# Kernel tuning notes

Hardware: AMD Instinct MI355X
Metric: run time of the kernel (lower is better)

## Reference

```python
import jax, jax.numpy as jnp
import numpy as np

M = 8192          # sketch width
TAU = 64.0
D = 3             # Chebyshev order
SIGMA_DP = 0.01


def setup_inputs() -> dict:
    key = jax.random.key(0)
    ks = jax.random.split(key, 8)
    B, C, K = 512, 4096, 1000
    x = jax.random.normal(ks[0], (B, C), dtype=jnp.float32)
    sketch_mu = jax.random.normal(ks[1], (C, M), dtype=jnp.float32) * 0.1
    g = jnp.where(jax.random.uniform(ks[2], (C,)) < 0.5, -1.0, 1.0).astype(jnp.float32)
    noise = jax.random.normal(ks[3], (C, M), dtype=jnp.float32)
    W = jax.random.normal(ks[4], (C, K), dtype=jnp.float32) * 0.02
    b = jax.random.normal(ks[5], (K,), dtype=jnp.float32) * 0.02
    h = jax.random.randint(ks[6], (C,), 0, M, dtype=jnp.int32)
    t = 10
    return {"x": x, "sketch_mu": sketch_mu, "g": g, "noise": noise,
            "W": W, "b": b, "h": h, "t": t}


def reference(x, sketch_mu, g, noise, W, b, h, t):
    tf = jnp.float32(t)
    lambda_t = 1.0 - jnp.exp(-tf / TAU)
    kappa_t = 1.0 / tf
    # hashed count-sketch scatter-add, vectorized over the batch:
    # per sample i: sketch_mu[:, h] += kappa * (g * x[i])[:, None]
    # under add semantics == kappa * outer(g * sum_i x[i], bincount(h))
    counts = jnp.zeros((M,), dtype=x.dtype).at[h].add(1.0)        # [m]
    update = kappa_t * (g * x.sum(axis=0))[:, None] * counts[None, :]  # [C, m]
    sk = sketch_mu * (1.0 - lambda_t) + update + SIGMA_DP * noise
    # moment estimation
    mu_hat = jnp.mean(sk * g[:, None], axis=1)                    # [C]
    var_hat = jnp.ones_like(mu_hat)
    skew_hat = jnp.zeros_like(mu_hat)
    kurt_hat = jnp.full_like(mu_hat, 3.0)
    # Chebyshev normalization (d = 3 -> all branches active)
    xn = (x - mu_hat) / (jnp.sqrt(var_hat) + 1e-6)
    if D >= 2:
        xn = xn - 0.5 * skew_hat * (xn ** 2 - 1.0)
    if D >= 3:
        xn = xn / jnp.sqrt(kurt_hat / 8.0 + 1e-6)
    # classifier head
    return xn @ W + b
```

## Files before the change

kernel.cpp:

```cpp
#include <hip/hip_runtime.h>
#include <hip/hip_bf16.h>


#define SPLITK 8

typedef float f32x4 __attribute__((ext_vector_type(4)));
typedef short bf16x8 __attribute__((ext_vector_type(8)));

__device__ __forceinline__ short f2bf(float f) {
    unsigned u = __float_as_uint(f);
    unsigned r = (u + 0x7FFFu + ((u >> 16) & 1u)) >> 16;
    return (short)r;
}
__device__ __forceinline__ float bf2f(short b) {
    return __uint_as_float(((unsigned)(unsigned short)b) << 16);
}

__global__ __launch_bounds__(256) void colsum_kernel(const float* __restrict__ x,
                                                     float* __restrict__ colsum,
                                                     int Cdim) {
    int c = blockIdx.x * 256 + threadIdx.x;
    const float* p = x + (size_t)(blockIdx.y * 8) * Cdim + c;
    float r0 = p[0 * (size_t)Cdim];
    float r1 = p[1 * (size_t)Cdim];
    float r2 = p[2 * (size_t)Cdim];
    float r3 = p[3 * (size_t)Cdim];
    float r4 = p[4 * (size_t)Cdim];
    float r5 = p[5 * (size_t)Cdim];
    float r6 = p[6 * (size_t)Cdim];
    float r7 = p[7 * (size_t)Cdim];
    __builtin_amdgcn_sched_barrier(0);
    float acc = ((r0 + r1) + (r2 + r3)) + ((r4 + r5) + (r6 + r7));
    atomicAdd(&colsum[c], acc);
}

__global__ __launch_bounds__(256, 4) void rowsum_kernel(const float* __restrict__ sk,
                                                        const float* __restrict__ noise,
                                                        const float* __restrict__ g,
                                                        const float* __restrict__ colsum,
                                                        const int* __restrict__ t_ptr,
                                                        float* __restrict__ mu,
                                                        int Msk, float hcount) {
    int row = blockIdx.x;
    int tid = threadIdx.x;
    const f32x4* ps = reinterpret_cast<const f32x4*>(sk + (size_t)row * Msk);
    const f32x4* pn = reinterpret_cast<const f32x4*>(noise + (size_t)row * Msk);
    int n4 = Msk >> 2;

    float ss = 0.0f, sn = 0.0f;
    int base = 0;
    for (; base + 2048 <= n4; base += 2048) {
        const f32x4* qs = ps + base + tid;
        const f32x4* qn = pn + base + tid;
        f32x4 a0 = __builtin_nontemporal_load(qs + 0 * 256);
        f32x4 a1 = __builtin_nontemporal_load(qs + 1 * 256);
        f32x4 a2 = __builtin_nontemporal_load(qs + 2 * 256);
        f32x4 a3 = __builtin_nontemporal_load(qs + 3 * 256);
        f32x4 a4 = __builtin_nontemporal_load(qs + 4 * 256);
        f32x4 a5 = __builtin_nontemporal_load(qs + 5 * 256);
        f32x4 a6 = __builtin_nontemporal_load(qs + 6 * 256);
        f32x4 a7 = __builtin_nontemporal_load(qs + 7 * 256);
        f32x4 b0 = __builtin_nontemporal_load(qn + 0 * 256);
        f32x4 b1 = __builtin_nontemporal_load(qn + 1 * 256);
        f32x4 b2 = __builtin_nontemporal_load(qn + 2 * 256);
        f32x4 b3 = __builtin_nontemporal_load(qn + 3 * 256);
        f32x4 b4 = __builtin_nontemporal_load(qn + 4 * 256);
        f32x4 b5 = __builtin_nontemporal_load(qn + 5 * 256);
        f32x4 b6 = __builtin_nontemporal_load(qn + 6 * 256);
        f32x4 b7 = __builtin_nontemporal_load(qn + 7 * 256);
        __builtin_amdgcn_sched_barrier(0);
        float s0 = (a0.x + a0.y) + (a0.z + a0.w);
        float s1 = (a1.x + a1.y) + (a1.z + a1.w);
        float s2 = (a2.x + a2.y) + (a2.z + a2.w);
        float s3 = (a3.x + a3.y) + (a3.z + a3.w);
        float s4 = (a4.x + a4.y) + (a4.z + a4.w);
        float s5 = (a5.x + a5.y) + (a5.z + a5.w);
        float s6 = (a6.x + a6.y) + (a6.z + a6.w);
        float s7 = (a7.x + a7.y) + (a7.z + a7.w);
        float t0 = (b0.x + b0.y) + (b0.z + b0.w);
        float t1 = (b1.x + b1.y) + (b1.z + b1.w);
        float t2 = (b2.x + b2.y) + (b2.z + b2.w);
        float t3 = (b3.x + b3.y) + (b3.z + b3.w);
        float t4 = (b4.x + b4.y) + (b4.z + b4.w);
        float t5 = (b5.x + b5.y) + (b5.z + b5.w);
        float t6 = (b6.x + b6.y) + (b6.z + b6.w);
        float t7 = (b7.x + b7.y) + (b7.z + b7.w);
        ss += ((s0 + s1) + (s2 + s3)) + ((s4 + s5) + (s6 + s7));
        sn += ((t0 + t1) + (t2 + t3)) + ((t4 + t5) + (t6 + t7));
    }
    for (int i = base + tid; i < n4; i += 256) {
        f32x4 v = ps[i];
        f32x4 w = pn[i];
        ss += (v.x + v.y) + (v.z + v.w);
        sn += (w.x + w.y) + (w.z + w.w);
    }

#pragma unroll
    for (int off = 32; off > 0; off >>= 1) {
        ss += __shfl_down(ss, off);
        sn += __shfl_down(sn, off);
    }
    __shared__ float red[2][4];
    int wid = tid >> 6;
    if ((tid & 63) == 0) { red[0][wid] = ss; red[1][wid] = sn; }
    __syncthreads();
    if (tid == 0) {
        float sst = (red[0][0] + red[0][1]) + (red[0][2] + red[0][3]);
        float snt = (red[1][0] + red[1][1]) + (red[1][2] + red[1][3]);
        float t = (float)(*t_ptr);
        float decay = __expf(-t / 64.0f);
        float kappa = 1.0f / t;
        float gc = g[row];
        float acc = decay * sst + 0.01f * snt;
        mu[row] = gc / (float)Msk * (acc + kappa * gc * colsum[row] * hcount);
    }
}

__global__ __launch_bounds__(256) void init_out_kernel(const float* __restrict__ bias,
                                                       float* __restrict__ out,
                                                       int Kdim, int total) {
    int i = blockIdx.x * 256 + threadIdx.x;
    if (i < total) out[i] = bias[i % Kdim];
}

template <bool ATOMIC>
__global__ __launch_bounds__(256, 4) void gemm_kernel(const float* __restrict__ x,
                                                      const float* __restrict__ W,
                                                      const float* __restrict__ mu,
                                                      float* __restrict__ outp,
                                                      int Bdim, int Cdim, int Kdim,
                                                      int Kc, float s) {
    __shared__ short As[2][64][40];
    __shared__ short Bs[2][64][40];

    const int tid = threadIdx.x;
    const int lane = tid & 63;
    const int w = tid >> 6;
    const int wr = w >> 1;
    const int wc = w & 1;
    const int row0 = blockIdx.x * 64;
    const int col0 = blockIdx.y * 64;
    const int cbeg = blockIdx.z * Kc;

    const int am = tid >> 2;
    const int ac8 = (tid & 3) * 8;
    const int bn = tid & 63;
    const int bk8 = (tid >> 6) * 8;
    const int bcol = col0 + bn;
    const bool bok = bcol < Kdim;

    const int fr = lane & 15;
    const int fk8 = (lane >> 4) * 8;

    f32x4 acc[2][2] = {};

    for (int it = 0; it < Kc; it += 32) {
        const int c0 = cbeg + it;
        const float* xr = &x[(size_t)(row0 + am) * Cdim + c0 + ac8];
        f32x4 xa = *reinterpret_cast<const f32x4*>(xr);
        f32x4 xb = *reinterpret_cast<const f32x4*>(xr + 4);
        f32x4 ma = *reinterpret_cast<const f32x4*>(&mu[c0 + ac8]);
        f32x4 mb = *reinterpret_cast<const f32x4*>(&mu[c0 + ac8 + 4]);
        float wv[8];
#pragma unroll
        for (int j = 0; j < 8; ++j)
            wv[j] = bok ? W[(size_t)(c0 + bk8 + j) * Kdim + bcol] : 0.0f;

        __syncthreads();

        float av[8];
        av[0] = s * (xa.x - ma.x); av[1] = s * (xa.y - ma.y);
        av[2] = s * (xa.z - ma.z); av[3] = s * (xa.w - ma.w);
        av[4] = s * (xb.x - mb.x); av[5] = s * (xb.y - mb.y);
        av[6] = s * (xb.z - mb.z); av[7] = s * (xb.w - mb.w);
        bf16x8 ah, al;
#pragma unroll
        for (int j = 0; j < 8; ++j) {
            short h = f2bf(av[j]);
            ah[j] = h;
            al[j] = f2bf(av[j] - bf2f(h));
        }
        *reinterpret_cast<bf16x8*>(&As[0][am][ac8]) = ah;
        *reinterpret_cast<bf16x8*>(&As[1][am][ac8]) = al;

        bf16x8 bh, bl;
#pragma unroll
        for (int j = 0; j < 8; ++j) {
            short h = f2bf(wv[j]);
            bh[j] = h;
            bl[j] = f2bf(wv[j] - bf2f(h));
        }
        *reinterpret_cast<bf16x8*>(&Bs[0][bn][bk8]) = bh;
        *reinterpret_cast<bf16x8*>(&Bs[1][bn][bk8]) = bl;

        __syncthreads();

        bf16x8 afr[2][2], bfr[2][2];
#pragma unroll
        for (int h = 0; h < 2; ++h) {
#pragma unroll
            for (int f = 0; f < 2; ++f) {
                afr[h][f] = *reinterpret_cast<const bf16x8*>(
                    &As[h][wr * 32 + f * 16 + fr][fk8]);
                bfr[h][f] = *reinterpret_cast<const bf16x8*>(
                    &Bs[h][wc * 32 + f * 16 + fr][fk8]);
            }
        }

#pragma unroll
        for (int mf = 0; mf < 2; ++mf) {
#pragma unroll
            for (int nf = 0; nf < 2; ++nf) {
                acc[mf][nf] = __builtin_amdgcn_mfma_f32_16x16x32_bf16(
                    afr[0][mf], bfr[0][nf], acc[mf][nf], 0, 0, 0);
                acc[mf][nf] = __builtin_amdgcn_mfma_f32_16x16x32_bf16(
                    afr[0][mf], bfr[1][nf], acc[mf][nf], 0, 0, 0);
                acc[mf][nf] = __builtin_amdgcn_mfma_f32_16x16x32_bf16(
                    afr[1][mf], bfr[0][nf], acc[mf][nf], 0, 0, 0);
            }
        }
    }

#pragma unroll
    for (int mf = 0; mf < 2; ++mf) {
#pragma unroll
        for (int nf = 0; nf < 2; ++nf) {
#pragma unroll
            for (int r = 0; r < 4; ++r) {
                int row = row0 + wr * 32 + mf * 16 + (lane >> 4) * 4 + r;
                int col = col0 + wc * 32 + nf * 16 + (lane & 15);
                if (col < Kdim) {
                    if (ATOMIC)
                        atomicAdd(&outp[(size_t)row * Kdim + col], acc[mf][nf][r]);
                    else
                        outp[((size_t)blockIdx.z * Bdim + row) * Kdim + col] =
                            acc[mf][nf][r];
                }
            }
        }
    }
}

__global__ __launch_bounds__(256) void reduce_kernel(const float* __restrict__ part,
                                                     const float* __restrict__ bias,
                                                     float* __restrict__ out,
                                                     int total4, int Kdim, int perz) {
    int i = blockIdx.x * 256 + threadIdx.x;
    if (i >= total4) return;
    const float4* p4 = reinterpret_cast<const float4*>(part);
    float4 sum = p4[i];
#pragma unroll
    for (int z = 1; z < SPLITK; ++z) {
        float4 v = p4[(size_t)z * (perz >> 2) + i];
        sum.x += v.x; sum.y += v.y; sum.z += v.z; sum.w += v.w;
    }
    int e = i * 4;
    sum.x += bias[(e + 0) % Kdim];
    sum.y += bias[(e + 1) % Kdim];
    sum.z += bias[(e + 2) % Kdim];
    sum.w += bias[(e + 3) % Kdim];
    reinterpret_cast<float4*>(out)[i] = sum;
}

extern "C" void kernel_launch(void* const* d_in, const int* in_sizes, int n_in,
                              void* d_out, int out_size, void* d_ws, size_t ws_size,
                              hipStream_t stream) {
    const float* x      = (const float*)d_in[0];
    const float* sk     = (const float*)d_in[1];
    const float* g      = (const float*)d_in[2];
    const float* noise  = (const float*)d_in[3];
    const float* W      = (const float*)d_in[4];
    const float* bias   = (const float*)d_in[5];
    const int* t_ptr    = (const int*)d_in[7];

    int C    = in_sizes[2];
    int Bdim = in_sizes[0] / C;
    int Msk  = in_sizes[1] / C;
    int Kdim = in_sizes[5];
    float hcount = (float)in_sizes[6];

    float* colsum = (float*)d_ws;
    float* mu     = colsum + C;
    float* part   = mu + C;

    size_t need = (size_t)(2 * C + SPLITK * Bdim * Kdim) * sizeof(float);
    bool use_partial = ws_size >= need;

    float s = (float)(1.0 / ((1.0 + 1e-6) * sqrt(0.375 + 1e-6)));
    int Kc = C / SPLITK;

    hipMemsetAsync(colsum, 0, C * sizeof(float), stream);
    {
        dim3 grid(C / 256, Bdim / 8);
        colsum_kernel<<<grid, 256, 0, stream>>>(x, colsum, C);
    }
    rowsum_kernel<<<C, 256, 0, stream>>>(sk, noise, g, colsum, t_ptr, mu, Msk, hcount);
    dim3 ggrid(Bdim / 64, (Kdim + 63) / 64, SPLITK);
    if (use_partial) {
        gemm_kernel<false><<<ggrid, 256, 0, stream>>>(x, W, mu, part, Bdim, C, Kdim,
                                                      Kc, s);
        int perz = Bdim * Kdim;
        int total4 = perz / 4;
        reduce_kernel<<<(total4 + 255) / 256, 256, 0, stream>>>(part, bias,
                                                                (float*)d_out,
                                                                total4, Kdim, perz);
    } else {
        int total = Bdim * Kdim;
        init_out_kernel<<<(total + 255) / 256, 256, 0, stream>>>(bias, (float*)d_out,
                                                                 Kdim, total);
        gemm_kernel<true><<<ggrid, 256, 0, stream>>>(x, W, mu, (float*)d_out, Bdim, C,
                                                     Kdim, Kc, s);
    }
}
```

Baseline: 313.3 us.

## Decouple mean subtraction from GEMM via GEMV and pre-split bf16 operands

Rewrites the normalized GEMM as s*(x@W) - s*(mu@W) + b, so mu now enters through a separate GEMV folded into the final reduce. This lets x and W be split into bf16 hi/lo once, in standalone kernels, instead of inside the GEMM inner loop. The rowsum is also split across two grid slices, one for the sketch and one for the noise, combined by atomics, to raise parallelism. The cost is extra workspace traffic and launches, and a slight change in rounding from subtracting mu after the product.

```diff
diff --git a/kernel.cpp b/kernel.cpp
--- a/kernel.cpp
+++ b/kernel.cpp
@@ -14,6 +14,25 @@
 }
 __device__ __forceinline__ float bf2f(short b) {
     return __uint_as_float(((unsigned)(unsigned short)b) << 16);
+}
+
+__global__ __launch_bounds__(256) void split_kernel(const float* __restrict__ src,
+                                                    short* __restrict__ hi,
+                                                    short* __restrict__ lo) {
+    int i = blockIdx.x * 256 + threadIdx.x;
+    const f32x4* p = reinterpret_cast<const f32x4*>(src) + 2 * (size_t)i;
+    f32x4 a = p[0];
+    f32x4 b = p[1];
+    float v[8] = {a.x, a.y, a.z, a.w, b.x, b.y, b.z, b.w};
+    bf16x8 h, l;
+#pragma unroll
+    for (int j = 0; j < 8; ++j) {
+        short hh = f2bf(v[j]);
+        h[j] = hh;
+        l[j] = f2bf(v[j] - bf2f(hh));
+    }
+    reinterpret_cast<bf16x8*>(hi)[i] = h;
+    reinterpret_cast<bf16x8*>(lo)[i] = l;
 }
 
 __global__ __launch_bounds__(256) void colsum_kernel(const float* __restrict__ x,
@@ -36,38 +55,27 @@
 
 __global__ __launch_bounds__(256, 4) void rowsum_kernel(const float* __restrict__ sk,
                                                         const float* __restrict__ noise,
-                                                        const float* __restrict__ g,
-                                                        const float* __restrict__ colsum,
                                                         const int* __restrict__ t_ptr,
-                                                        float* __restrict__ mu,
-                                                        int Msk, float hcount) {
+                                                        float* __restrict__ accrow,
+                                                        int Msk) {
     int row = blockIdx.x;
     int tid = threadIdx.x;
-    const f32x4* ps = reinterpret_cast<const f32x4*>(sk + (size_t)row * Msk);
-    const f32x4* pn = reinterpret_cast<const f32x4*>(noise + (size_t)row * Msk);
+    const float* src = (blockIdx.y == 0) ? sk : noise;
+    const f32x4* p = reinterpret_cast<const f32x4*>(src + (size_t)row * Msk);
     int n4 = Msk >> 2;
 
-    float ss = 0.0f, sn = 0.0f;
+    float sum = 0.0f;
     int base = 0;
     for (; base + 2048 <= n4; base += 2048) {
-        const f32x4* qs = ps + base + tid;
-        const f32x4* qn = pn + base + tid;
-        f32x4 a0 = __builtin_nontemporal_load(qs + 0 * 256);
-        f32x4 a1 = __builtin_nontemporal_load(qs + 1 * 256);
-        f32x4 a2 = __builtin_nontemporal_load(qs + 2 * 256);
-        f32x4 a3 = __builtin_nontemporal_load(qs + 3 * 256);
-        f32x4 a4 = __builtin_nontemporal_load(qs + 4 * 256);
-        f32x4 a5 = __builtin_nontemporal_load(qs + 5 * 256);
-        f32x4 a6 = __builtin_nontemporal_load(qs + 6 * 256);
-        f32x4 a7 = __builtin_nontemporal_load(qs + 7 * 256);
-        f32x4 b0 = __builtin_nontemporal_load(qn + 0 * 256);
-        f32x4 b1 = __builtin_nontemporal_load(qn + 1 * 256);
-        f32x4 b2 = __builtin_nontemporal_load(qn + 2 * 256);
-        f32x4 b3 = __builtin_nontemporal_load(qn + 3 * 256);
-        f32x4 b4 = __builtin_nontemporal_load(qn + 4 * 256);
-        f32x4 b5 = __builtin_nontemporal_load(qn + 5 * 256);
-        f32x4 b6 = __builtin_nontemporal_load(qn + 6 * 256);
-        f32x4 b7 = __builtin_nontemporal_load(qn + 7 * 256);
+        const f32x4* q = p + base + tid;
+        f32x4 a0 = __builtin_nontemporal_load(q + 0 * 256);
+        f32x4 a1 = __builtin_nontemporal_load(q + 1 * 256);
+        f32x4 a2 = __builtin_nontemporal_load(q + 2 * 256);
+        f32x4 a3 = __builtin_nontemporal_load(q + 3 * 256);
+        f32x4 a4 = __builtin_nontemporal_load(q + 4 * 256);
+        f32x4 a5 = __builtin_nontemporal_load(q + 5 * 256);
+        f32x4 a6 = __builtin_nontemporal_load(q + 6 * 256);
+        f32x4 a7 = __builtin_nontemporal_load(q + 7 * 256);
         __builtin_amdgcn_sched_barrier(0);
         float s0 = (a0.x + a0.y) + (a0.z + a0.w);
         float s1 = (a1.x + a1.y) + (a1.z + a1.w);
@@ -77,56 +85,87 @@
         float s5 = (a5.x + a5.y) + (a5.z + a5.w);
         float s6 = (a6.x + a6.y) + (a6.z + a6.w);
         float s7 = (a7.x + a7.y) + (a7.z + a7.w);
-        float t0 = (b0.x + b0.y) + (b0.z + b0.w);
-        float t1 = (b1.x + b1.y) + (b1.z + b1.w);
-        float t2 = (b2.x + b2.y) + (b2.z + b2.w);
-        float t3 = (b3.x + b3.y) + (b3.z + b3.w);
-        float t4 = (b4.x + b4.y) + (b4.z + b4.w);
-        float t5 = (b5.x + b5.y) + (b5.z + b5.w);
-        float t6 = (b6.x + b6.y) + (b6.z + b6.w);
-        float t7 = (b7.x + b7.y) + (b7.z + b7.w);
-        ss += ((s0 + s1) + (s2 + s3)) + ((s4 + s5) + (s6 + s7));
-        sn += ((t0 + t1) + (t2 + t3)) + ((t4 + t5) + (t6 + t7));
+        sum += ((s0 + s1) + (s2 + s3)) + ((s4 + s5) + (s6 + s7));
     }
     for (int i = base + tid; i < n4; i += 256) {
-        f32x4 v = ps[i];
-        f32x4 w = pn[i];
-        ss += (v.x + v.y) + (v.z + v.w);
-        sn += (w.x + w.y) + (w.z + w.w);
-    }
-
-#pragma unroll
-    for (int off = 32; off > 0; off >>= 1) {
-        ss += __shfl_down(ss, off);
-        sn += __shfl_down(sn, off);
-    }
-    __shared__ float red[2][4];
+        f32x4 v = p[i];
+        sum += (v.x + v.y) + (v.z + v.w);
+    }
+
+#pragma unroll
+    for (int off = 32; off > 0; off >>= 1)
+        sum += __shfl_down(sum, off);
+
+    __shared__ float red[4];
     int wid = tid >> 6;
-    if ((tid & 63) == 0) { red[0][wid] = ss; red[1][wid] = sn; }
+    if ((tid & 63) == 0) red[wid] = sum;
     __syncthreads();
     if (tid == 0) {
-        float sst = (red[0][0] + red[0][1]) + (red[0][2] + red[0][3]);
-        float snt = (red[1][0] + red[1][1]) + (red[1][2] + red[1][3]);
-        float t = (float)(*t_ptr);
-        float decay = __expf(-t / 64.0f);
-        float kappa = 1.0f / t;
-        float gc = g[row];
-        float acc = decay * sst + 0.01f * snt;
-        mu[row] = gc / (float)Msk * (acc + kappa * gc * colsum[row] * hcount);
+        float total = (red[0] + red[1]) + (red[2] + red[3]);
+        float w;
+        if (blockIdx.y == 0) {
+            float t = (float)(*t_ptr);
+            w = __expf(-t / 64.0f);
+        } else {
+            w = 0.01f;
+        }
+        atomicAdd(&accrow[row], w * total);
+    }
+}
+
+__global__ __launch_bounds__(256) void gemv_kernel(const float* __restrict__ W,
+                                                   const float* __restrict__ accrow,
+                                                   const float* __restrict__ colsum,
+                                                   const float* __restrict__ g,
+                                                   const int* __restrict__ t_ptr,
+                                                   float* __restrict__ v,
+                                                   int Cdim, int Kdim, int Msk,
+                                                   float hcount) {
+    int tid = threadIdx.x;
+    int lane = tid & 63;
+    int w = tid >> 6;
+    int k = blockIdx.x * 64 + lane;
+    bool kok = k < Kdim;
+    int cbase = blockIdx.y * 128 + w * 32;
+
+    float t = (float)(*t_ptr);
+    float kap_h = hcount / t;
+    float invM = 1.0f / (float)Msk;
+
+    float sum = 0.0f;
+    for (int c = cbase; c < cbase + 32; ++c) {
+        float gc = g[c];
+        float mu_c = gc * invM * (accrow[c] + kap_h * gc * colsum[c]);
+        float wv = kok ? W[(size_t)c * Kdim + k] : 0.0f;
+        sum += mu_c * wv;
+    }
+
+    __shared__ float part[4][64];
+    part[w][lane] = sum;
+    __syncthreads();
+    if (w == 0 && kok) {
+        float total = (part[0][lane] + part[1][lane]) +
+                      (part[2][lane] + part[3][lane]);
+        atomicAdd(&v[k], total);
     }
 }
 
 __global__ __launch_bounds__(256) void init_out_kernel(const float* __restrict__ bias,
+                                                       const float* __restrict__ v,
                                                        float* __restrict__ out,
-                                                       int Kdim, int total) {
+                                                       int Kdim, int total, float s) {
     int i = blockIdx.x * 256 + threadIdx.x;
-    if (i < total) out[i] = bias[i % Kdim];
+    if (i < total) {
+        int k = i % Kdim;
+        out[i] = bias[k] - s * v[k];
+    }
 }
 
 template <bool ATOMIC>
-__global__ __launch_bounds__(256, 4) void gemm_kernel(const float* __restrict__ x,
-                                                      const float* __restrict__ W,
-                                                      const float* __restrict__ mu,
+__global__ __launch_bounds__(256, 4) void gemm_kernel(const short* __restrict__ xhi,
+                                                      const short* __restrict__ xlo,
+                                                      const short* __restrict__ whi,
+                                                      const short* __restrict__ wlo,
                                                       float* __restrict__ outp,
                                                       int Bdim, int Cdim, int Kdim,
                                                       int Kc, float s) {
@@ -156,42 +195,26 @@
 
     for (int it = 0; it < Kc; it += 32) {
         const int c0 = cbeg + it;
-        const float* xr = &x[(size_t)(row0 + am) * Cdim + c0 + ac8];
-        f32x4 xa = *reinterpret_cast<const f32x4*>(xr);
-        f32x4 xb = *reinterpret_cast<const f32x4*>(xr + 4);
-        f32x4 ma = *reinterpret_cast<const f32x4*>(&mu[c0 + ac8]);
-        f32x4 mb = *reinterpret_cast<const f32x4*>(&mu[c0 + ac8 + 4]);
-        float wv[8];
-#pragma unroll
-        for (int j = 0; j < 8; ++j)
-            wv[j] = bok ? W[(size_t)(c0 + bk8 + j) * Kdim + bcol] : 0.0f;
+        const size_t aoff = (size_t)(row0 + am) * Cdim + c0 + ac8;
+        bf16x8 ah = *reinterpret_cast<const bf16x8*>(&xhi[aoff]);
+        bf16x8 al = *reinterpret_cast<const bf16x8*>(&xlo[aoff]);
+        short bh[8], bl[8];
+#pragma unroll
+        for (int j = 0; j < 8; ++j) {
+            size_t woff = (size_t)(c0 + bk8 + j) * Kdim + bcol;
+            bh[j] = bok ? whi[woff] : (short)0;
+            bl[j] = bok ? wlo[woff] : (short)0;
+        }
 
         __syncthreads();
 
-        float av[8];
-        av[0] = s * (xa.x - ma.x); av[1] = s * (xa.y - ma.y);
-        av[2] = s * (xa.z - ma.z); av[3] = s * (xa.w - ma.w);
-        av[4] = s * (xb.x - mb.x); av[5] = s * (xb.y - mb.y);
-        av[6] = s * (xb.z - mb.z); av[7] = s * (xb.w - mb.w);
-        bf16x8 ah, al;
-#pragma unroll
-        for (int j = 0; j < 8; ++j) {
-            short h = f2bf(av[j]);
-            ah[j] = h;
-            al[j] = f2bf(av[j] - bf2f(h));
-        }
         *reinterpret_cast<bf16x8*>(&As[0][am][ac8]) = ah;
         *reinterpret_cast<bf16x8*>(&As[1][am][ac8]) = al;
-
-        bf16x8 bh, bl;
-#pragma unroll
-        for (int j = 0; j < 8; ++j) {
-            short h = f2bf(wv[j]);
-            bh[j] = h;
-            bl[j] = f2bf(wv[j] - bf2f(h));
-        }
-        *reinterpret_cast<bf16x8*>(&Bs[0][bn][bk8]) = bh;
-        *reinterpret_cast<bf16x8*>(&Bs[1][bn][bk8]) = bl;
+        bf16x8 bhv, blv;
+#pragma unroll
+        for (int j = 0; j < 8; ++j) { bhv[j] = bh[j]; blv[j] = bl[j]; }
+        *reinterpret_cast<bf16x8*>(&Bs[0][bn][bk8]) = bhv;
+        *reinterpret_cast<bf16x8*>(&Bs[1][bn][bk8]) = blv;
 
         __syncthreads();
 
@@ -231,7 +254,8 @@
                 int col = col0 + wc * 32 + nf * 16 + (lane & 15);
                 if (col < Kdim) {
                     if (ATOMIC)
-                        atomicAdd(&outp[(size_t)row * Kdim + col], acc[mf][nf][r]);
+                        atomicAdd(&outp[(size_t)row * Kdim + col],
+                                  s * acc[mf][nf][r]);
                     else
                         outp[((size_t)blockIdx.z * Bdim + row) * Kdim + col] =
                             acc[mf][nf][r];
@@ -243,23 +267,28 @@
 
 __global__ __launch_bounds__(256) void reduce_kernel(const float* __restrict__ part,
                                                      const float* __restrict__ bias,
+                                                     const float* __restrict__ v,
                                                      float* __restrict__ out,
-                                                     int total4, int Kdim, int perz) {
+                                                     int total4, int Kdim, int perz,
+                                                     float s) {
     int i = blockIdx.x * 256 + threadIdx.x;
     if (i >= total4) return;
     const float4* p4 = reinterpret_cast<const float4*>(part);
     float4 sum = p4[i];
 #pragma unroll
     for (int z = 1; z < SPLITK; ++z) {
-        float4 v = p4[(size_t)z * (perz >> 2) + i];
-        sum.x += v.x; sum.y += v.y; sum.z += v.z; sum.w += v.w;
+        float4 vv = p4[(size_t)z * (perz >> 2) + i];
+        sum.x += vv.x; sum.y += vv.y; sum.z += vv.z; sum.w += vv.w;
     }
     int e = i * 4;
-    sum.x += bias[(e + 0) % Kdim];
-    sum.y += bias[(e + 1) % Kdim];
-    sum.z += bias[(e + 2) % Kdim];
-    sum.w += bias[(e + 3) % Kdim];
-    reinterpret_cast<float4*>(out)[i] = sum;
+    int k0 = (e + 0) % Kdim, k1 = (e + 1) % Kdim;
+    int k2 = (e + 2) % Kdim, k3 = (e + 3) % Kdim;
+    float4 o;
+    o.x = s * (sum.x - v[k0]) + bias[k0];
+    o.y = s * (sum.y - v[k1]) + bias[k1];
+    o.z = s * (sum.z - v[k2]) + bias[k2];
+    o.w = s * (sum.w - v[k3]) + bias[k3];
+    reinterpret_cast<float4*>(out)[i] = o;
 }
 
 extern "C" void kernel_launch(void* const* d_in, const int* in_sizes, int n_in,
@@ -280,35 +309,55 @@
     float hcount = (float)in_sizes[6];
 
     float* colsum = (float*)d_ws;
-    float* mu     = colsum + C;
-    float* part   = mu + C;
-
-    size_t need = (size_t)(2 * C + SPLITK * Bdim * Kdim) * sizeof(float);
+    float* accrow = colsum + C;
+    float* v      = accrow + C;
+    char* base    = (char*)(v + 1024);
+    size_t xcnt = (size_t)Bdim * C;
+    size_t wcnt = (size_t)C * Kdim;
+    short* xhi = (short*)base;
+    short* xlo = xhi + xcnt;
+    short* whi = xlo + xcnt;
+    short* wlo = whi + wcnt;
+    float* part = (float*)(wlo + wcnt);
+
+    size_t need = (size_t)((char*)(part + (size_t)SPLITK * Bdim * Kdim) - (char*)d_ws);
     bool use_partial = ws_size >= need;
 
     float s = (float)(1.0 / ((1.0 + 1e-6) * sqrt(0.375 + 1e-6)));
     int Kc = C / SPLITK;
 
-    hipMemsetAsync(colsum, 0, C * sizeof(float), stream);
+    hipMemsetAsync(colsum, 0, (2 * C + 1024) * sizeof(float), stream);
+    split_kernel<<<(int)(xcnt / 8 / 256), 256, 0, stream>>>(x, xhi, xlo);
+    split_kernel<<<(int)(wcnt / 8 / 256), 256, 0, stream>>>(W, whi, wlo);
     {
         dim3 grid(C / 256, Bdim / 8);
         colsum_kernel<<<grid, 256, 0, stream>>>(x, colsum, C);
     }
-    rowsum_kernel<<<C, 256, 0, stream>>>(sk, noise, g, colsum, t_ptr, mu, Msk, hcount);
+    {
+        dim3 grid(C, 2);
+        rowsum_kernel<<<grid, 256, 0, stream>>>(sk, noise, t_ptr, accrow, Msk);
+    }
     dim3 ggrid(Bdim / 64, (Kdim + 63) / 64, SPLITK);
+    dim3 vgrid((Kdim + 63) / 64, 32);
     if (use_partial) {
-        gemm_kernel<false><<<ggrid, 256, 0, stream>>>(x, W, mu, part, Bdim, C, Kdim,
-                                                      Kc, s);
+        gemm_kernel<false><<<ggrid, 256, 0, stream>>>(xhi, xlo, whi, wlo, part,
+                                                      Bdim, C, Kdim, Kc, s);
+        gemv_kernel<<<vgrid, 256, 0, stream>>>(W, accrow, colsum, g, t_ptr, v,
+                                               C, Kdim, Msk, hcount);
         int perz = Bdim * Kdim;
         int total4 = perz / 4;
-        reduce_kernel<<<(total4 + 255) / 256, 256, 0, stream>>>(part, bias,
+        reduce_kernel<<<(total4 + 255) / 256, 256, 0, stream>>>(part, bias, v,
                                                                 (float*)d_out,
-                                                                total4, Kdim, perz);
+                                                                total4, Kdim, perz, s);
     } else {
+        gemv_kernel<<<vgrid, 256, 0, stream>>>(W, accrow, colsum, g, t_ptr, v,
+                                               C, Kdim, Msk, hcount);
         int total = Bdim * Kdim;
-        init_out_kernel<<<(total + 255) / 256, 256, 0, stream>>>(bias, (float*)d_out,
-                                                                 Kdim, total);
-        gemm_kernel<true><<<ggrid, 256, 0, stream>>>(x, W, mu, (float*)d_out, Bdim, C,
-                                                     Kdim, Kc, s);
-    }
-}
+        init_out_kernel<<<(total + 255) / 256, 256, 0, stream>>>(bias, v,
+                                                                 (float*)d_out,
+                                                                 Kdim, total, s);
+        gemm_kernel<true><<<ggrid, 256, 0, stream>>>(xhi, xlo, whi, wlo,
+                                                     (float*)d_out, Bdim, C, Kdim,
+                                                     Kc, s);
+    }
+}
```

Measured after the change: 329.9 us. +5.3%, slower.
